# Performance work log

Hardware: AMD Instinct MI355X
Metric: run time of the kernel (lower is better)

Reference implementation:

```python
import jax, jax.numpy as jnp
import numpy as np

DK = 8.0          # sqrt(in_dim) with in_dim = 64
BN_SCALE = 1.0 / np.float32(np.sqrt(1.0 + 1e-5))  # eval-mode BatchNorm3d at init (mean=0, var=1, gamma=1, beta=0)


def conv3d(x, w, b):
    # x: [B,Cin,D1,D2,D3], w: [Cout,Cin,3,3,3], stride 1, padding 1 == SAME
    y = jax.lax.conv_general_dilated(
        x, w, window_strides=(1, 1, 1), padding='SAME',
        dimension_numbers=('NCDHW', 'OIDHW', 'NCDHW'))
    return y + b[None, :, None, None, None]


def axial(qm, km, vm):
    # qm/km/vm: [B,C,S,L,M]; attention over L with keys along M-contraction.
    # scores[b,c,s,i,j] = sum_m (q/dk)[...,i,m] * k[...,j,m]  -> [B,C,S,L,L]
    s = jnp.einsum('bcsim,bcsjm->bcsij', qm / DK, km)
    # torch nn.Softmax(dim=1) applied to [N,L,L] normalizes over the FIRST L axis (i)
    a = jax.nn.softmax(s, axis=-2)
    return jnp.einsum('bcsij,bcsjm->bcsim', a, vm)


def setup_inputs() -> dict:
    key = jax.random.key(0)
    ks = jax.random.split(key, 5)
    B, C, H, W, D = 2, 64, 64, 64, 64
    x = jax.random.normal(ks[0], (B, C, H, W, D), jnp.float32)
    Wq = jax.random.normal(ks[1], (C, C, 3, 3, 3), jnp.float32) * 0.02
    Wk = jax.random.normal(ks[2], (C, C, 3, 3, 3), jnp.float32) * 0.02
    Wv = jax.random.normal(ks[3], (C, C, 3, 3, 3), jnp.float32) * 0.02
    Wc = jax.random.normal(ks[4], (C, 3 * C, 3, 3, 3), jnp.float32) * 0.02
    z = jnp.zeros((C,), jnp.float32)
    return {"x": x, "Wq": Wq, "bq": z, "Wk": Wk, "bk": z,
            "Wv": Wv, "bv": z, "Wc": Wc, "bc": z}


def reference(x, Wq, bq, Wk, bk, Wv, bv, Wc, bc):
    # projections (dropout is inactive at inference)
    q = conv3d(x, Wq, bq)
    k = conv3d(x, Wk, bk)
    v = conv3d(x, Wv, bv)
    P = jnp.transpose

    # ---- loop over D slices: attend over H (and over W in the transposed pass) ----
    pa = (0, 1, 4, 2, 3)        # [B,C,D,H,W]
    ava = axial(P(q, pa), P(k, pa), P(v, pa))          # [B,C,D,H,W]
    ava = P(ava, (0, 1, 3, 4, 2))                       # -> [B,C,H,W,D]
    pb = (0, 1, 4, 3, 2)        # [B,C,D,W,H]
    ava1 = axial(P(q, pb), P(k, pb), P(v, pb))          # [B,C,D,W,H]
    ava1 = P(ava1, (0, 1, 4, 3, 2))                     # -> [B,C,H,W,D]
    AVa = (ava + ava1) * 0.5

    # ---- loop over W slices: attend over H (and over D) ----
    pc = (0, 1, 3, 2, 4)        # [B,C,W,H,D]
    avb = axial(P(q, pc), P(k, pc), P(v, pc))           # [B,C,W,H,D]
    avb = P(avb, (0, 1, 3, 2, 4))                       # -> [B,C,H,W,D]
    pd = (0, 1, 3, 4, 2)        # [B,C,W,D,H]
    avb1 = axial(P(q, pd), P(k, pd), P(v, pd))          # [B,C,W,D,H]
    avb1 = P(avb1, (0, 1, 4, 2, 3))                     # -> [B,C,H,W,D]
    AVb = (avb + avb1) * 0.5

    # ---- loop over H slices: attend over W (and over D) ----
    avc = axial(q, k, v)                                 # [B,C,H,W,D]
    pe = (0, 1, 2, 4, 3)        # [B,C,H,D,W]
    avc1 = axial(P(q, pe), P(k, pe), P(v, pe))          # [B,C,H,D,W]
    avc1 = P(avc1, (0, 1, 2, 4, 3))                     # -> [B,C,H,W,D]
    AVc = (avc + avc1) * 0.5

    cat = jnp.concatenate([AVa, AVb, AVc], axis=1)      # [B,3C,H,W,D]
    y = jax.nn.relu(conv3d(cat, Wc, bc) * BN_SCALE)     # Conv_3x3x3: conv + BN(eval) + ReLU
    y = y * BN_SCALE                                    # outer BatchNorm3d (eval)
    return y + q
```

## Files before the change

### kernel.cpp

```cpp
#include <hip/hip_runtime.h>

typedef unsigned short u16;
typedef unsigned int u32;
typedef __attribute__((ext_vector_type(8))) __bf16 bf16x8;
typedef __attribute__((ext_vector_type(4))) float f32x4;
typedef __attribute__((ext_vector_type(4))) u16 u16x4;

#define VOL 262144

__device__ __forceinline__ u16 f2bf(float f) {
  u32 u = __builtin_bit_cast(u32, f);
  u32 r = u + 0x7FFFu + ((u >> 16) & 1u);
  return (u16)(r >> 16);
}
__device__ __forceinline__ float bf2f(u16 h) {
  return __builtin_bit_cast(float, ((u32)h) << 16);
}
__device__ __forceinline__ bf16x8 ldsfrag(const u16* p) { return *(const bf16x8*)p; }

__device__ __forceinline__ int swA(int row, int col) {
  return row * 64 + (col ^ (((row ^ (row >> 3)) & 7) << 3));
}

__global__ __launch_bounds__(256) void swz_qkv(const float* __restrict__ Wq,
    const float* __restrict__ Wk, const float* __restrict__ Wv, u16* __restrict__ out) {
  int idx = blockIdx.x * 256 + threadIdx.x;
  if (idx >= 54 * 12 * 64 * 8) return;
  int jj = idx & 7;
  int lane = (idx >> 3) & 63;
  int t = idx >> 9;
  int nf = t % 12, s = t / 12;
  int dh = s / 18, sub = s % 18;
  int dw = sub / 6, dd = (sub >> 1) % 3, c32 = sub & 1;
  int coutg = nf * 16 + (lane & 15);
  int cin = c32 * 32 + (lane >> 4) * 8 + jj;
  const float* W = (coutg < 64) ? Wq : ((coutg < 128) ? Wk : Wv);
  int c = coutg & 63;
  out[idx] = f2bf(W[(c * 64 + cin) * 27 + dh * 9 + dw * 3 + dd]);
}

__global__ __launch_bounds__(256) void swz_c(const float* __restrict__ Wc, u16* __restrict__ out) {
  int idx = blockIdx.x * 256 + threadIdx.x;
  if (idx >= 162 * 4 * 64 * 8) return;
  int jj = idx & 7;
  int lane = (idx >> 3) & 63;
  int nf = (idx >> 9) & 3;
  int s = idx >> 11;
  int dh = s / 54, rem = s % 54;
  int t = rem / 18, sub = rem % 18;
  int dw = sub / 6, dd = (sub >> 1) % 3, c32 = sub & 1;
  int cout = nf * 16 + (lane & 15);
  int cin = t * 64 + c32 * 32 + (lane >> 4) * 8 + jj;
  out[idx] = f2bf(Wc[(cout * 192 + cin) * 27 + dh * 9 + dw * 3 + dd]);
}

__global__ __launch_bounds__(512, 2) void conv_qkv(const float* __restrict__ x,
    const u16* __restrict__ BQ, const float* __restrict__ bq, const float* __restrict__ bk,
    const float* __restrict__ bv, u16* __restrict__ qb, u16* __restrict__ kb,
    u16* __restrict__ vb) {
  __shared__ __align__(16) u16 xT[4 * 66 * 72];
  int tid = threadIdx.x;
  int id = blockIdx.x;
  int lin = (id & 7) * 512 + (id >> 3);
  int b = lin >> 11, h = (lin >> 5) & 63, w0 = (lin & 31) * 2;
  int wave = tid >> 6, lane = tid & 63, r = lane & 15, g = lane >> 4;
  int mhalf = wave >> 2, nq = wave & 3;
  int pairid = tid >> 3, seg = tid & 7;
  if (tid < 256) {
    int wwi = tid >> 6, ci = tid & 63;
    xT[(wwi * 66 + 0) * 72 + ci] = 0;
    xT[(wwi * 66 + 65) * 72 + ci] = 0;
  }
  f32x4 acc[4][3];
#pragma unroll
  for (int i = 0; i < 4; ++i)
#pragma unroll
    for (int j = 0; j < 3; ++j)
#pragma unroll
      for (int e = 0; e < 4; ++e) acc[i][j][e] = 0.0f;

  for (int dh = 0; dh < 3; ++dh) {
    int hh = h + dh - 1;
    if ((unsigned)hh >= 64u) continue;
    __syncthreads();
#pragma unroll
    for (int pi = 0; pi < 2; ++pi) {
      int pair = pairid + 64 * pi;
      int wwi = pair >> 5, cin0 = (pair & 31) * 2;
      int ww = w0 + wwi - 1;
      float4 a0{}, a1{}, b0{}, b1{};
      if ((unsigned)ww < 64u) {
        const float* p = x + (size_t)(b * 64 + cin0) * VOL + hh * 4096 + ww * 64 + seg * 8;
        a0 = *(const float4*)p;        a1 = *(const float4*)(p + 4);
        b0 = *(const float4*)(p + VOL); b1 = *(const float4*)(p + VOL + 4);
      }
      u16 ua[8], ub[8];
      ua[0]=f2bf(a0.x); ua[1]=f2bf(a0.y); ua[2]=f2bf(a0.z); ua[3]=f2bf(a0.w);
      ua[4]=f2bf(a1.x); ua[5]=f2bf(a1.y); ua[6]=f2bf(a1.z); ua[7]=f2bf(a1.w);
      ub[0]=f2bf(b0.x); ub[1]=f2bf(b0.y); ub[2]=f2bf(b0.z); ub[3]=f2bf(b0.w);
      ub[4]=f2bf(b1.x); ub[5]=f2bf(b1.y); ub[6]=f2bf(b1.z); ub[7]=f2bf(b1.w);
      int rowb = wwi * 66;
#pragma unroll
      for (int di = 0; di < 8; ++di) {
        int dpos = seg * 8 + di + 1;
        *(u32*)&xT[(rowb + dpos) * 72 + (cin0 ^ (((dpos >> 3) & 7) << 3))] =
            (u32)ua[di] | ((u32)ub[di] << 16);
      }
    }
    __syncthreads();
    for (int sub = 0; sub < 18; ++sub) {
      int dw = sub / 6, dd = (sub >> 1) % 3, c32 = sub & 1;
      int colb = c32 * 32 + g * 8;
      int wwi = mhalf + dw;
      bf16x8 A[4];
#pragma unroll
      for (int l = 0; l < 4; ++l) {
        int dpos = l * 16 + r + dd;
        A[l] = ldsfrag(&xT[(wwi * 66 + dpos) * 72 + (colb ^ (((dpos >> 3) & 7) << 3))]);
      }
      const u16* Bp = BQ + ((size_t)((dh * 18 + sub) * 12 + nq * 3) * 64 + lane) * 8;
#pragma unroll
      for (int nf = 0; nf < 3; ++nf) {
        bf16x8 Bf = *(const bf16x8*)(Bp + nf * 512);
#pragma unroll
        for (int l = 0; l < 4; ++l)
          acc[l][nf] = __builtin_amdgcn_mfma_f32_16x16x32_bf16(A[l], Bf, acc[l][nf], 0, 0, 0);
      }
    }
  }
#pragma unroll
  for (int nf = 0; nf < 3; ++nf) {
    int coutg = (nq * 3 + nf) * 16 + r;
    int ten = coutg >> 6, c = coutg & 63;
    u16* dst = (ten == 0) ? qb : ((ten == 1) ? kb : vb);
    const float* bias = (ten == 0) ? bq : ((ten == 1) ? bk : bv);
    float bsv = bias[c];
#pragma unroll
    for (int l = 0; l < 4; ++l) {
      int d0 = l * 16 + g * 4;
      int idx = (b * 64 + c) * VOL + h * 4096 + (w0 + mhalf) * 64 + d0;
      u16x4 o;
#pragma unroll
      for (int jj = 0; jj < 4; ++jj) o[jj] = f2bf(acc[l][nf][jj] + bsv);
      *(u16x4*)(dst + idx) = o;
    }
  }
}

__global__ __launch_bounds__(256, 6) void ktranspose(const u16* __restrict__ src,
    u16* __restrict__ dst, int P, int Q) {
  __shared__ __align__(16) u16 tile[64 * 72];
  int tid = threadIdx.x;
  int id = blockIdx.x;
  int bc = id >> 6, t = id & 63;
  int qt = Q >> 6;
  int p0 = (t / qt) * 64, q0 = (t % qt) * 64;
  const u16* s = src + (size_t)bc * VOL;
  u16* d = dst + (size_t)bc * VOL;
#pragma unroll
  for (int it = 0; it < 2; ++it) {
    int c = tid + 256 * it;
    int i2 = c >> 3, sg = c & 7;
    *(uint4*)&tile[i2 * 72 + ((sg * 8) ^ (((i2 >> 3) & 7) << 3))] =
        *(const uint4*)&s[(size_t)(p0 + i2) * Q + q0 + sg * 8];
  }
  __syncthreads();
  int j = tid >> 2, ms = tid & 3;
  u16 vals[16];
#pragma unroll
  for (int ii = 0; ii < 16; ++ii) {
    int row = ms * 16 + ii;
    vals[ii] = tile[row * 72 + (j ^ (((row >> 3) & 7) << 3))];
  }
  uint4 o0, o1;
  o0.x = (u32)vals[0] | ((u32)vals[1] << 16);
  o0.y = (u32)vals[2] | ((u32)vals[3] << 16);
  o0.z = (u32)vals[4] | ((u32)vals[5] << 16);
  o0.w = (u32)vals[6] | ((u32)vals[7] << 16);
  o1.x = (u32)vals[8] | ((u32)vals[9] << 16);
  o1.y = (u32)vals[10] | ((u32)vals[11] << 16);
  o1.z = (u32)vals[12] | ((u32)vals[13] << 16);
  o1.w = (u32)vals[14] | ((u32)vals[15] << 16);
  size_t drow = (size_t)(q0 + j) * P + p0 + ms * 16;
  *(uint4*)&d[drow] = o0;
  *(uint4*)&d[drow + 8] = o1;
}

__global__ __launch_bounds__(256, 2) void attn_pair(const u16* __restrict__ q,
    const u16* __restrict__ k, const u16* __restrict__ v, u16* __restrict__ dst,
    int uStride, int sMul) {
  __shared__ __align__(16) u16 sm[6 * 4096];
  u16* LQ = sm;             u16* LK = sm + 4096;      u16* LV = sm + 2 * 4096;
  u16* LQT = sm + 3 * 4096; u16* LKT = sm + 4 * 4096; u16* LVT = sm + 5 * 4096;
  u16* A1 = LK;
  u16* A2 = LKT;
  int tid = threadIdx.x;
  int id = blockIdx.x;
  int bc = id >> 6, sidx = id & 63;
  size_t base = (size_t)bc * VOL + (size_t)sidx * sMul;
  int wave = tid >> 6, lane = tid & 63, r = lane & 15, g = lane >> 4;
  int pairid = tid >> 3, seg = tid & 7;
  int u0 = pairid * 2;
  const u16* srcs[3] = {q, k, v};
  u16* Ln_[3] = {LQ, LK, LV};
  u16* Lt_[3] = {LQT, LKT, LVT};
#pragma unroll
  for (int t3 = 0; t3 < 3; ++t3) {
    const u16* p = srcs[t3] + base + (size_t)u0 * uStride + seg * 8;
    uint4 ra = *(const uint4*)p;
    uint4 rb = *(const uint4*)(p + uStride);
    *(uint4*)&Ln_[t3][swA(u0, seg * 8)] = ra;
    *(uint4*)&Ln_[t3][swA(u0 + 1, seg * 8)] = rb;
    union { uint4 vv; u16 ss[8]; } Ua, Ub;
    Ua.vv = ra; Ub.vv = rb;
#pragma unroll
    for (int vi = 0; vi < 8; ++vi) {
      int vvx = seg * 8 + vi;
      *(u32*)&Lt_[t3][swA(vvx, u0)] = (u32)Ua.ss[vi] | ((u32)Ub.ss[vi] << 16);
    }
  }
  __syncthreads();
  int row0 = wave * 16;
  f32x4 s1[4], s2[4];
#pragma unroll
  for (int nf = 0; nf < 4; ++nf)
#pragma unroll
    for (int e = 0; e < 4; ++e) { s1[nf][e] = 0.f; s2[nf][e] = 0.f; }
#pragma unroll
  for (int ks = 0; ks < 2; ++ks) {
    int cb = ks * 32 + g * 8;
    bf16x8 aK = ldsfrag(&LK[swA(row0 + r, cb)]);
    bf16x8 aKT = ldsfrag(&LKT[swA(row0 + r, cb)]);
#pragma unroll
    for (int nf = 0; nf < 4; ++nf) {
      bf16x8 bQ = ldsfrag(&LQ[swA(nf * 16 + r, cb)]);
      bf16x8 bQT = ldsfrag(&LQT[swA(nf * 16 + r, cb)]);
      s1[nf] = __builtin_amdgcn_mfma_f32_16x16x32_bf16(aK, bQ, s1[nf], 0, 0, 0);
      s2[nf] = __builtin_amdgcn_mfma_f32_16x16x32_bf16(aKT, bQT, s2[nf], 0, 0, 0);
    }
  }
  __syncthreads();
#pragma unroll
  for (int m2 = 0; m2 < 2; ++m2) {
    f32x4* ss = m2 ? s2 : s1;
    u16* Adst = m2 ? A2 : A1;
#pragma unroll
    for (int jj = 0; jj < 4; ++jj) {
      float mx = fmaxf(fmaxf(ss[0][jj], ss[1][jj]), fmaxf(ss[2][jj], ss[3][jj]));
      mx = fmaxf(mx, __shfl_xor(mx, 1, 64));
      mx = fmaxf(mx, __shfl_xor(mx, 2, 64));
      mx = fmaxf(mx, __shfl_xor(mx, 4, 64));
      mx = fmaxf(mx, __shfl_xor(mx, 8, 64));
      float p0 = __expf((ss[0][jj] - mx) * 0.125f);
      float p1 = __expf((ss[1][jj] - mx) * 0.125f);
      float p2 = __expf((ss[2][jj] - mx) * 0.125f);
      float p3 = __expf((ss[3][jj] - mx) * 0.125f);
      float sum = p0 + p1 + p2 + p3;
      sum += __shfl_xor(sum, 1, 64);
      sum += __shfl_xor(sum, 2, 64);
      sum += __shfl_xor(sum, 4, 64);
      sum += __shfl_xor(sum, 8, 64);
      float inv = 1.0f / sum;
      ss[0][jj] = p0 * inv; ss[1][jj] = p1 * inv; ss[2][jj] = p2 * inv; ss[3][jj] = p3 * inv;
    }
    int j0 = row0 + g * 4;
#pragma unroll
    for (int nf = 0; nf < 4; ++nf) {
      int i = nf * 16 + r;
      int a0 = swA(i, j0);
      *(u32*)&Adst[a0]     = (u32)f2bf(ss[nf][0]) | ((u32)f2bf(ss[nf][1]) << 16);
      *(u32*)&Adst[a0 + 2] = (u32)f2bf(ss[nf][2]) | ((u32)f2bf(ss[nf][3]) << 16);
    }
  }
  __syncthreads();
  f32x4 o[4];
#pragma unroll
  for (int nf = 0; nf < 4; ++nf)
#pragma unroll
    for (int e = 0; e < 4; ++e) o[nf][e] = 0.f;
#pragma unroll
  for (int ks = 0; ks < 2; ++ks) {
    int cb = ks * 32 + g * 8;
    bf16x8 aA = ldsfrag(&A1[swA(row0 + r, cb)]);
    bf16x8 aV = ldsfrag(&LV[swA(row0 + r, cb)]);
#pragma unroll
    for (int nf = 0; nf < 4; ++nf) {
      bf16x8 bVT = ldsfrag(&LVT[swA(nf * 16 + r, cb)]);
      bf16x8 bA2 = ldsfrag(&A2[swA(nf * 16 + r, cb)]);
      o[nf] = __builtin_amdgcn_mfma_f32_16x16x32_bf16(aA, bVT, o[nf], 0, 0, 0);
      o[nf] = __builtin_amdgcn_mfma_f32_16x16x32_bf16(aV, bA2, o[nf], 0, 0, 0);
    }
  }
#pragma unroll
  for (int nf = 0; nf < 4; ++nf) {
    int vv = nf * 16 + r;
#pragma unroll
    for (int jj = 0; jj < 4; ++jj) {
      int u = row0 + g * 4 + jj;
      dst[base + (size_t)u * uStride + vv] = f2bf(o[nf][jj] * 0.5f);
    }
  }
}

__global__ __launch_bounds__(512, 2) void conv_final(const u16* __restrict__ AVa,
    const u16* __restrict__ AVb, const u16* __restrict__ AVc, const u16* __restrict__ BCw,
    const float* __restrict__ bcb, const u16* __restrict__ qb, float* __restrict__ out) {
  __shared__ __align__(16) u16 xT[6 * 66 * 72];
  int tid = threadIdx.x;
  int id = blockIdx.x;
  int lin = (id & 7) * 256 + (id >> 3);
  int b = lin >> 10, h = (lin >> 4) & 63, w0 = (lin & 15) * 4;
  int wave = tid >> 6, lane = tid & 63, r = lane & 15, g = lane >> 4;
  int mw = wave >> 1, nw = wave & 1;
  int pairid = tid >> 3, seg = tid & 7;
  if (tid < 384) {
    int wwi = tid >> 6, ci = tid & 63;
    xT[(wwi * 66 + 0) * 72 + ci] = 0;
    xT[(wwi * 66 + 65) * 72 + ci] = 0;
  }
  f32x4 acc[4][2];
#pragma unroll
  for (int i = 0; i < 4; ++i)
#pragma unroll
    for (int j = 0; j < 2; ++j)
#pragma unroll
      for (int e = 0; e < 4; ++e) acc[i][j][e] = 0.f;

  for (int dh = 0; dh < 3; ++dh) {
    int hh = h + dh - 1;
    if ((unsigned)hh >= 64u) continue;
    for (int t = 0; t < 3; ++t) {
      const u16* sp = (t == 0) ? AVa : ((t == 1) ? AVb : AVc);
      __syncthreads();
#pragma unroll
      for (int pi = 0; pi < 3; ++pi) {
        int pair = pairid + 64 * pi;
        int wwi = pair >> 5, cin0 = (pair & 31) * 2;
        int ww = w0 + wwi - 1;
        uint4 ra{}, rb{};
        if ((unsigned)ww < 64u) {
          const u16* p = sp + (size_t)(b * 64 + cin0) * VOL + hh * 4096 + ww * 64 + seg * 8;
          ra = *(const uint4*)p;
          rb = *(const uint4*)(p + VOL);
        }
        union { uint4 vv; u16 ss[8]; } Ua, Ub;
        Ua.vv = ra; Ub.vv = rb;
        int rowb = wwi * 66;
#pragma unroll
        for (int di = 0; di < 8; ++di) {
          int dpos = seg * 8 + di + 1;
          *(u32*)&xT[(rowb + dpos) * 72 + (cin0 ^ (((dpos >> 3) & 7) << 3))] =
              (u32)Ua.ss[di] | ((u32)Ub.ss[di] << 16);
        }
      }
      __syncthreads();
      for (int sub = 0; sub < 18; ++sub) {
        int dw = sub / 6, dd = (sub >> 1) % 3, c32 = sub & 1;
        int colb = c32 * 32 + g * 8;
        int wwi = mw + dw;
        bf16x8 A[4];
#pragma unroll
        for (int dq = 0; dq < 4; ++dq) {
          int dpos = dq * 16 + r + dd;
          A[dq] = ldsfrag(&xT[(wwi * 66 + dpos) * 72 + (colb ^ (((dpos >> 3) & 7) << 3))]);
        }
        const u16* Bp = BCw + ((size_t)(((dh * 3 + t) * 18 + sub) * 4 + nw * 2) * 64 + lane) * 8;
#pragma unroll
        for (int nf = 0; nf < 2; ++nf) {
          bf16x8 Bf = *(const bf16x8*)(Bp + nf * 512);
#pragma unroll
          for (int dq = 0; dq < 4; ++dq)
            acc[dq][nf] = __builtin_amdgcn_mfma_f32_16x16x32_bf16(A[dq], Bf, acc[dq][nf], 0, 0, 0);
        }
      }
    }
  }
  const float S = 0.9999950000374997f;
#pragma unroll
  for (int nf = 0; nf < 2; ++nf) {
    int cout = (nw * 2 + nf) * 16 + r;
    float bsv = bcb[cout];
#pragma unroll
    for (int dq = 0; dq < 4; ++dq) {
      int d0 = dq * 16 + g * 4;
      int idx = (b * 64 + cout) * VOL + h * 4096 + (w0 + mw) * 64 + d0;
      u16x4 qv = *(const u16x4*)(qb + idx);
      float4 ov;
      float t0 = (acc[dq][nf][0] + bsv) * S; t0 = t0 > 0.f ? t0 : 0.f; ov.x = t0 * S + bf2f(qv[0]);
      float t1 = (acc[dq][nf][1] + bsv) * S; t1 = t1 > 0.f ? t1 : 0.f; ov.y = t1 * S + bf2f(qv[1]);
      float t2 = (acc[dq][nf][2] + bsv) * S; t2 = t2 > 0.f ? t2 : 0.f; ov.z = t2 * S + bf2f(qv[2]);
      float t3 = (acc[dq][nf][3] + bsv) * S; t3 = t3 > 0.f ? t3 : 0.f; ov.w = t3 * S + bf2f(qv[3]);
      *(float4*)(out + idx) = ov;
    }
  }
}

extern "C" void kernel_launch(void* const* d_in, const int* in_sizes, int n_in,
                              void* d_out, int out_size, void* d_ws, size_t ws_size,
                              hipStream_t stream) {
  const float* x  = (const float*)d_in[0];
  const float* Wq = (const float*)d_in[1];
  const float* bq = (const float*)d_in[2];
  const float* Wk = (const float*)d_in[3];
  const float* bk = (const float*)d_in[4];
  const float* Wv = (const float*)d_in[5];
  const float* bv = (const float*)d_in[6];
  const float* Wc = (const float*)d_in[7];
  const float* bc = (const float*)d_in[8];
  float* out = (float*)d_out;
  u16* ws = (u16*)d_ws;
  const size_t T = (size_t)33554432;
  u16* qb = ws;
  u16* kb = ws + T;
  u16* vb = ws + 2 * T;
  u16* qT = ws + 3 * T;
  u16* kT = ws + 4 * T;
  u16* vT = ws + 5 * T;
  u16* avaT = ws + 6 * T;
  u16* BQ = ws + 7 * T;
  u16* BC = BQ + 331776;
  u16* AVa = qT;
  u16* AVb = kT;
  u16* AVc = vT;

  swz_qkv<<<1296, 256, 0, stream>>>(Wq, Wk, Wv, BQ);
  swz_c<<<1296, 256, 0, stream>>>(Wc, BC);
  conv_qkv<<<4096, 512, 0, stream>>>(x, BQ, bq, bk, bv, qb, kb, vb);
  ktranspose<<<8192, 256, 0, stream>>>(qb, qT, 4096, 64);
  ktranspose<<<8192, 256, 0, stream>>>(kb, kT, 4096, 64);
  ktranspose<<<8192, 256, 0, stream>>>(vb, vT, 4096, 64);
  attn_pair<<<8192, 256, 0, stream>>>(qT, kT, vT, avaT, 64, 4096);
  ktranspose<<<8192, 256, 0, stream>>>(avaT, AVa, 64, 4096);
  attn_pair<<<8192, 256, 0, stream>>>(qb, kb, vb, AVb, 4096, 64);
  attn_pair<<<8192, 256, 0, stream>>>(qb, kb, vb, AVc, 64, 4096);
  conv_final<<<2048, 512, 0, stream>>>(AVa, AVb, AVc, BC, bc, qb, out);
}
```

Measured before the change: 1.011 ms.

## Pre-convert input to bf16 channel-last and double-buffer conv_qkv loads via global_load_lds

A new xcvt kernel converts the fp32 NCDHW input once into a bf16 channels-last, pre-swizzled layout. conv_qkv then streams each h-slice straight into LDS with direct global-to-LDS 16-byte loads. These loads are double-buffered so the next dh slice is fetched while MFMAs run on the current one. This is meant to remove the per-tile fp32 reads, conversions and LDS scatter stores from the conv hot loop and to overlap memory with compute. It costs an extra pass over the input and doubles the LDS footprint, which may reduce occupancy. It also relies on the avaT workspace being free before attention runs, since xcl reuses that region.

```diff
diff --git a/kernel.cpp b/kernel.cpp
--- a/kernel.cpp
+++ b/kernel.cpp
@@ -17,6 +17,12 @@
   return __builtin_bit_cast(float, ((u32)h) << 16);
 }
 __device__ __forceinline__ bf16x8 ldsfrag(const u16* p) { return *(const bf16x8*)p; }
+
+__device__ __forceinline__ void gload16(const u16* g, u16* l) {
+  __builtin_amdgcn_global_load_lds(
+      (const __attribute__((address_space(1))) u32*)g,
+      (__attribute__((address_space(3))) u32*)l, 16, 0, 0);
+}
 
 __device__ __forceinline__ int swA(int row, int col) {
   return row * 64 + (col ^ (((row ^ (row >> 3)) & 7) << 3));
@@ -54,23 +60,60 @@
   out[idx] = f2bf(Wc[(cout * 192 + cin) * 27 + dh * 9 + dw * 3 + dd]);
 }
 
-__global__ __launch_bounds__(512, 2) void conv_qkv(const float* __restrict__ x,
+__global__ __launch_bounds__(256, 4) void xcvt(const float* __restrict__ x, u16* __restrict__ xcl) {
+  __shared__ __align__(16) u16 tile[4096];
+  int id = blockIdx.x;
+  int b = id >> 12;
+  int t = threadIdx.x;
+  int c0 = (t & 31) * 2, d0 = (t >> 5) * 8;
+  const float* p0 = x + (size_t)(b * 64 + c0) * VOL + (size_t)(id & 4095) * 64 + d0;
+  float4 r00 = *(const float4*)p0;
+  float4 r01 = *(const float4*)(p0 + 4);
+  float4 r10 = *(const float4*)(p0 + VOL);
+  float4 r11 = *(const float4*)(p0 + VOL + 4);
+  float a0[8] = {r00.x, r00.y, r00.z, r00.w, r01.x, r01.y, r01.z, r01.w};
+  float a1[8] = {r10.x, r10.y, r10.z, r10.w, r11.x, r11.y, r11.z, r11.w};
+#pragma unroll
+  for (int i = 0; i < 8; ++i) {
+    int d = d0 + i;
+    *(u32*)&tile[d * 64 + (c0 ^ ((d & 7) << 3))] =
+        (u32)f2bf(a0[i]) | ((u32)f2bf(a1[i]) << 16);
+  }
+  __syncthreads();
+  u16* dst = xcl + ((size_t)id << 12);
+  *(uint4*)&dst[t * 16] = *(const uint4*)&tile[t * 16];
+  *(uint4*)&dst[t * 16 + 8] = *(const uint4*)&tile[t * 16 + 8];
+}
+
+__global__ __launch_bounds__(512, 2) void conv_qkv(const u16* __restrict__ xcl,
     const u16* __restrict__ BQ, const float* __restrict__ bq, const float* __restrict__ bk,
     const float* __restrict__ bv, u16* __restrict__ qb, u16* __restrict__ kb,
     u16* __restrict__ vb) {
-  __shared__ __align__(16) u16 xT[4 * 66 * 72];
+  __shared__ __align__(16) u16 xT[2 * 16896];
   int tid = threadIdx.x;
   int id = blockIdx.x;
   int lin = (id & 7) * 512 + (id >> 3);
   int b = lin >> 11, h = (lin >> 5) & 63, w0 = (lin & 31) * 2;
   int wave = tid >> 6, lane = tid & 63, r = lane & 15, g = lane >> 4;
   int mhalf = wave >> 2, nq = wave & 3;
-  int pairid = tid >> 3, seg = tid & 7;
-  if (tid < 256) {
-    int wwi = tid >> 6, ci = tid & 63;
-    xT[(wwi * 66 + 0) * 72 + ci] = 0;
-    xT[(wwi * 66 + 65) * 72 + ci] = 0;
-  }
+  {
+    int tl = tid >> 7, rs = (tid >> 6) & 1, ci = tid & 63;
+    int off = tl * 4224 + rs * 65 * 64 + ci;
+    xT[off] = 0;
+    xT[16896 + off] = 0;
+  }
+  if (w0 == 0) {
+    *(uint4*)&xT[64 + tid * 8] = uint4{0, 0, 0, 0};
+    *(uint4*)&xT[16896 + 64 + tid * 8] = uint4{0, 0, 0, 0};
+  }
+  if (w0 == 62) {
+    *(uint4*)&xT[3 * 4224 + 64 + tid * 8] = uint4{0, 0, 0, 0};
+    *(uint4*)&xT[16896 + 3 * 4224 + 64 + tid * 8] = uint4{0, 0, 0, 0};
+  }
+  int tw = wave >> 1, half = wave & 1;
+  int wws = w0 + tw - 1;
+  bool doload = (unsigned)wws < 64u;
+
   f32x4 acc[4][3];
 #pragma unroll
   for (int i = 0; i < 4; ++i)
@@ -79,35 +122,27 @@
 #pragma unroll
       for (int e = 0; e < 4; ++e) acc[i][j][e] = 0.0f;
 
-  for (int dh = 0; dh < 3; ++dh) {
-    int hh = h + dh - 1;
-    if ((unsigned)hh >= 64u) continue;
+  int dhlo = (h == 0) ? 1 : 0, dhhi = (h == 63) ? 1 : 2;
+  if (doload) {
+    int hh = h + dhlo - 1;
+    const u16* gp = xcl + (((size_t)(b * 64 + hh) * 64 + wws) << 12) + (half << 11) + (lane << 3);
+    u16* lp = &xT[tw * 4224 + 64 + half * 2048];
+#pragma unroll
+    for (int j = 0; j < 4; ++j) gload16(gp + j * 512, lp + j * 512);
+  }
+  int cur = 0;
+  for (int dh = dhlo; dh <= dhhi; ++dh) {
     __syncthreads();
-#pragma unroll
-    for (int pi = 0; pi < 2; ++pi) {
-      int pair = pairid + 64 * pi;
-      int wwi = pair >> 5, cin0 = (pair & 31) * 2;
-      int ww = w0 + wwi - 1;
-      float4 a0{}, a1{}, b0{}, b1{};
-      if ((unsigned)ww < 64u) {
-        const float* p = x + (size_t)(b * 64 + cin0) * VOL + hh * 4096 + ww * 64 + seg * 8;
-        a0 = *(const float4*)p;        a1 = *(const float4*)(p + 4);
-        b0 = *(const float4*)(p + VOL); b1 = *(const float4*)(p + VOL + 4);
-      }
-      u16 ua[8], ub[8];
-      ua[0]=f2bf(a0.x); ua[1]=f2bf(a0.y); ua[2]=f2bf(a0.z); ua[3]=f2bf(a0.w);
-      ua[4]=f2bf(a1.x); ua[5]=f2bf(a1.y); ua[6]=f2bf(a1.z); ua[7]=f2bf(a1.w);
-      ub[0]=f2bf(b0.x); ub[1]=f2bf(b0.y); ub[2]=f2bf(b0.z); ub[3]=f2bf(b0.w);
-      ub[4]=f2bf(b1.x); ub[5]=f2bf(b1.y); ub[6]=f2bf(b1.z); ub[7]=f2bf(b1.w);
-      int rowb = wwi * 66;
-#pragma unroll
-      for (int di = 0; di < 8; ++di) {
-        int dpos = seg * 8 + di + 1;
-        *(u32*)&xT[(rowb + dpos) * 72 + (cin0 ^ (((dpos >> 3) & 7) << 3))] =
-            (u32)ua[di] | ((u32)ub[di] << 16);
-      }
-    }
-    __syncthreads();
+    if (dh < dhhi && doload) {
+      int hh = h + dh;
+      const u16* gp =
+          xcl + (((size_t)(b * 64 + hh) * 64 + wws) << 12) + (half << 11) + (lane << 3);
+      u16* lp = &xT[(cur ^ 1) * 16896 + tw * 4224 + 64 + half * 2048];
+#pragma unroll
+      for (int j = 0; j < 4; ++j) gload16(gp + j * 512, lp + j * 512);
+    }
+    const u16* Bbase = BQ + ((size_t)(dh * 18) * 12 + nq * 3) * 512 + (size_t)lane * 8;
+    int bufE = cur * 16896;
     for (int sub = 0; sub < 18; ++sub) {
       int dw = sub / 6, dd = (sub >> 1) % 3, c32 = sub & 1;
       int colb = c32 * 32 + g * 8;
@@ -116,9 +151,9 @@
 #pragma unroll
       for (int l = 0; l < 4; ++l) {
         int dpos = l * 16 + r + dd;
-        A[l] = ldsfrag(&xT[(wwi * 66 + dpos) * 72 + (colb ^ (((dpos >> 3) & 7) << 3))]);
+        A[l] = ldsfrag(&xT[bufE + wwi * 4224 + dpos * 64 + (colb ^ (((dpos - 1) & 7) << 3))]);
       }
-      const u16* Bp = BQ + ((size_t)((dh * 18 + sub) * 12 + nq * 3) * 64 + lane) * 8;
+      const u16* Bp = Bbase + (size_t)sub * 12 * 512;
 #pragma unroll
       for (int nf = 0; nf < 3; ++nf) {
         bf16x8 Bf = *(const bf16x8*)(Bp + nf * 512);
@@ -127,6 +162,7 @@
           acc[l][nf] = __builtin_amdgcn_mfma_f32_16x16x32_bf16(A[l], Bf, acc[l][nf], 0, 0, 0);
       }
     }
+    cur ^= 1;
   }
 #pragma unroll
   for (int nf = 0; nf < 3; ++nf) {
@@ -416,6 +452,7 @@
   u16* qT = ws + 3 * T;
   u16* kT = ws + 4 * T;
   u16* vT = ws + 5 * T;
+  u16* xcl = ws + 6 * T;
   u16* avaT = ws + 6 * T;
   u16* BQ = ws + 7 * T;
   u16* BC = BQ + 331776;
@@ -425,7 +462,8 @@
 
   swz_qkv<<<1296, 256, 0, stream>>>(Wq, Wk, Wv, BQ);
   swz_c<<<1296, 256, 0, stream>>>(Wc, BC);
-  conv_qkv<<<4096, 512, 0, stream>>>(x, BQ, bq, bk, bv, qb, kb, vb);
+  xcvt<<<8192, 256, 0, stream>>>(x, xcl);
+  conv_qkv<<<4096, 512, 0, stream>>>(xcl, BQ, bq, bk, bv, qb, kb, vb);
   ktranspose<<<8192, 256, 0, stream>>>(qb, qT, 4096, 64);
   ktranspose<<<8192, 256, 0, stream>>>(kb, kT, 4096, 64);
   ktranspose<<<8192, 256, 0, stream>>>(vb, vT, 4096, 64);
```

Measured after the change: 1.005 ms. No clear change (-0.5%).
